# Optimization experiments

Hardware: AMD Instinct MI355X
Metric: run time of the kernel (lower is better)

Reference implementation:

```python
import jax, jax.numpy as jnp
import numpy as np

N, E = 50000, 800000          # nodes, edges
IN, H, C = 256, 4, 64          # in_channels, heads, per-head out channels
HID, OUT = 64, 40              # lin1 hidden, num classes
NEG_SLOPE = 0.2                # PyG GATConv default


def setup_inputs() -> dict:
    key = jax.random.key(0)
    ks = jax.random.split(key, 10)
    s = 0.05
    return {
        "x": jax.random.normal(ks[0], (N, IN), jnp.float32),
        "edge_index": jax.random.randint(ks[1], (2, E), 0, N, dtype=jnp.int64),
        "W": jax.random.normal(ks[2], (IN, H * C), jnp.float32) * s,     # GATConv lin (no bias)
        "att_src": jax.random.normal(ks[3], (H, C), jnp.float32) * s,
        "att_dst": jax.random.normal(ks[4], (H, C), jnp.float32) * s,
        "bias_conv": jnp.zeros((H * C,), jnp.float32),
        "W1": jax.random.normal(ks[5], (H * C, HID), jnp.float32) * s,
        "b1": jnp.zeros((HID,), jnp.float32),
        "W2": jax.random.normal(ks[6], (HID, OUT), jnp.float32) * s,
        "b2": jnp.zeros((OUT,), jnp.float32),
    }


def reference(x, edge_index, W, att_src, att_dst, bias_conv, W1, b1, W2, b2):
    n = x.shape[0]
    # PyG GATConv default: add self-loops (also guarantees no empty segments)
    loop = jnp.arange(n, dtype=edge_index.dtype)
    src = jnp.concatenate([edge_index[0], loop])  # [E+N]
    dst = jnp.concatenate([edge_index[1], loop])

    h = (x @ W).reshape(n, H, C)                         # [N,H,C]
    a_src = jnp.einsum('nhc,hc->nh', h, att_src)         # [N,H]
    a_dst = jnp.einsum('nhc,hc->nh', h, att_dst)

    # per-edge attention logits + segment softmax over incoming edges of dst
    e = jax.nn.leaky_relu(a_src[src] + a_dst[dst], NEG_SLOPE)   # [E+N,H]
    m = jax.ops.segment_max(e, dst, num_segments=n)             # [N,H]
    ex = jnp.exp(e - m[dst])
    denom = jax.ops.segment_sum(ex, dst, num_segments=n)
    alpha = ex / denom[dst]                                     # [E+N,H]

    # weighted scatter-aggregate of source features
    msg = alpha[:, :, None] * h[src]                            # [E+N,H,C]
    out = jax.ops.segment_sum(msg, dst, num_segments=n)         # [N,H,C]
    out = out.reshape(n, H * C) + bias_conv

    out = jax.nn.relu(out)              # .relu() after conv1 (dropout off in eval)
    out = jax.nn.relu(out @ W1 + b1)    # lin1 + relu
    return out @ W2 + b2                # lin2
```

## Files before the change

kernel.cpp:

```cpp
#include <hip/hip_runtime.h>
#include <math.h>

#define HEADS 4
#define CH 64
#define HC 256
#define SLOPE 0.2f
#define SLOT 64

typedef __attribute__((ext_vector_type(8))) short bf16x8;
typedef __attribute__((ext_vector_type(8))) unsigned short u16x8;
typedef __attribute__((ext_vector_type(4))) float f32x4;

__device__ __forceinline__ float4 ld4(const float* p){ return *(const float4*)p; }
__device__ __forceinline__ void st4(float* p, float4 v){ *(float4*)p = v; }
__device__ __forceinline__ float lrelu(float x){ return x > 0.f ? x : SLOPE * x; }
__device__ __forceinline__ unsigned short f2bf(float f){
  union { float f; unsigned int u; } v; v.f = f;
  unsigned int r = v.u + 0x7fffu + ((v.u >> 16) & 1u);
  return (unsigned short)(r >> 16);
}
__device__ __forceinline__ float bflo(unsigned int u){
  union { unsigned int u; float f; } v; v.u = u << 16; return v.f;
}
__device__ __forceinline__ float bfhi(unsigned int u){
  union { unsigned int u; float f; } v; v.u = u & 0xffff0000u; return v.f;
}
__device__ __forceinline__ void split2(float v, unsigned short& h, unsigned short& l){
  unsigned int u = __float_as_uint(v);
  h = (unsigned short)(u >> 16);
  float hf = __uint_as_float(u & 0xffff0000u);
  l = (unsigned short)(__float_as_uint(v - hf) >> 16);
}
__device__ __forceinline__ void dma16(const unsigned short* g, unsigned short* l){
  __builtin_amdgcn_global_load_lds(
      (const __attribute__((address_space(1))) unsigned int*)g,
      (__attribute__((address_space(3))) unsigned int*)l, 16, 0, 0);
}

__global__ __launch_bounds__(256) void k_pre(
    const float* __restrict__ W, const float* __restrict__ W1, const float* __restrict__ W2,
    unsigned short* __restrict__ Bhi, unsigned short* __restrict__ Blo,
    unsigned short* __restrict__ W1h, unsigned short* __restrict__ W1l,
    unsigned short* __restrict__ W2h, unsigned short* __restrict__ W2l) {
  int b = blockIdx.x, t = threadIdx.x;
  if (b < 256) {
    int nn = b;
    unsigned short h, l;
    split2(W[(size_t)t*256 + nn], h, l);
    Bhi[(size_t)nn*256 + t] = h; Blo[(size_t)nn*256 + t] = l;
  } else if (b < 320) {
    int nn = b - 256;
    unsigned short h, l;
    split2(W1[(size_t)t*64 + nn], h, l);
    W1h[(size_t)nn*256 + t] = h; W1l[(size_t)nn*256 + t] = l;
  } else {
    if (t < 64) {
      int nn = b - 320;
      float v = (nn < 40) ? W2[(size_t)t*40 + nn] : 0.f;
      unsigned short h, l;
      split2(v, h, l);
      W2h[(size_t)nn*64 + t] = h; W2l[(size_t)nn*64 + t] = l;
    }
  }
}

__global__ __launch_bounds__(256, 4) void k_gemmfill(const float* __restrict__ x,
    const unsigned short* __restrict__ Bhi_t, const unsigned short* __restrict__ Blo_t,
    unsigned short* __restrict__ hbf,
    const float* __restrict__ att_src, const float* __restrict__ att_dst,
    float* __restrict__ a_srcO, float* __restrict__ a_dstO, int M, int nFill,
    const int* __restrict__ ei, int* __restrict__ cnt, int* __restrict__ csrf,
    int E, int EN) {
  __shared__ __align__(16) unsigned short L[4*4096];
  int t = threadIdx.x;
  int b = blockIdx.x;
  if (b < nFill) {
    int base = b*2048 + t;
    int s0=0,d0=0,s1=0,d1=0,s2=0,d2=0,s3=0,d3=0;
    int s4=0,d4=0,s5=0,d5=0,s6=0,d6=0,s7=0,d7=0;
    int e0=base, e1=base+256, e2=base+512, e3=base+768;
    int e4=base+1024, e5=base+1280, e6=base+1536, e7=base+1792;
    bool q0=e0<EN,q1=e1<EN,q2=e2<EN,q3=e3<EN,q4=e4<EN,q5=e5<EN,q6=e6<EN,q7=e7<EN;
    if (q0) { if (e0<E) { s0=ei[e0]; d0=ei[E+e0]; } else { s0=e0-E; d0=s0; } }
    if (q1) { if (e1<E) { s1=ei[e1]; d1=ei[E+e1]; } else { s1=e1-E; d1=s1; } }
    if (q2) { if (e2<E) { s2=ei[e2]; d2=ei[E+e2]; } else { s2=e2-E; d2=s2; } }
    if (q3) { if (e3<E) { s3=ei[e3]; d3=ei[E+e3]; } else { s3=e3-E; d3=s3; } }
    if (q4) { if (e4<E) { s4=ei[e4]; d4=ei[E+e4]; } else { s4=e4-E; d4=s4; } }
    if (q5) { if (e5<E) { s5=ei[e5]; d5=ei[E+e5]; } else { s5=e5-E; d5=s5; } }
    if (q6) { if (e6<E) { s6=ei[e6]; d6=ei[E+e6]; } else { s6=e6-E; d6=s6; } }
    if (q7) { if (e7<E) { s7=ei[e7]; d7=ei[E+e7]; } else { s7=e7-E; d7=s7; } }
    if (q0) { int p = atomicAdd(&cnt[d0], 1); csrf[(d0<<6) + p] = s0; }
    if (q1) { int p = atomicAdd(&cnt[d1], 1); csrf[(d1<<6) + p] = s1; }
    if (q2) { int p = atomicAdd(&cnt[d2], 1); csrf[(d2<<6) + p] = s2; }
    if (q3) { int p = atomicAdd(&cnt[d3], 1); csrf[(d3<<6) + p] = s3; }
    if (q4) { int p = atomicAdd(&cnt[d4], 1); csrf[(d4<<6) + p] = s4; }
    if (q5) { int p = atomicAdd(&cnt[d5], 1); csrf[(d5<<6) + p] = s5; }
    if (q6) { int p = atomicAdd(&cnt[d6], 1); csrf[(d6<<6) + p] = s6; }
    if (q7) { int p = atomicAdd(&cnt[d7], 1); csrf[(d7<<6) + p] = s7; }
    return;
  }
  int gb = b - nFill;
  int lane = t & 63, w = t >> 6;
  int wr = w >> 1, wc = w & 1;
  int ln15 = lane & 15, lq = lane >> 4;
  int row0 = (gb >> 1) * 128, col0 = (gb & 1) * 128;

  f32x4 acc[4][4];
  #pragma unroll
  for (int i=0;i<4;i++)
    #pragma unroll
    for (int j=0;j<4;j++) acc[i][j] = (f32x4){0.f,0.f,0.f,0.f};

  int sA = w*128 + lane;
  int sB = sA + 64;
  int RA = sA>>3, uA = (sA&7)^(RA&7), idxA = (RA<<1)|(uA&1), segA = uA>>1;
  int RB = sB>>3, uB = (sB&7)^(RB&7), idxB = (RB<<1)|(uB&1), segB = uB>>1;
  size_t gB_a = (size_t)(col0+idxA)*256 + segA*8;
  size_t gB_b = (size_t)(col0+idxB)*256 + segB*8;
  int l0 = (w*128)*8, l1 = (w*128+64)*8;

  int ar = t >> 1, akh = t & 1;
  int arow = row0 + ar;
  bool avalid = arow < M;
  const float* xp = &x[(size_t)arow*256 + akh*16];
  int aR = ar >> 1;
  int u0w = ((2*akh+0) << 1) | (ar & 1);
  int u1w = ((2*akh+1) << 1) | (ar & 1);
  int as0 = aR*8 + (u0w ^ (aR & 7));
  int as1 = aR*8 + (u1w ^ (aR & 7));

  for (int c = 0; c < 8; c++) {
    int k0 = c*32;
    dma16(Bhi_t + gB_a + k0, &L[2*4096 + l0]);
    dma16(Bhi_t + gB_b + k0, &L[2*4096 + l1]);
    dma16(Blo_t + gB_a + k0, &L[3*4096 + l0]);
    dma16(Blo_t + gB_b + k0, &L[3*4096 + l1]);
    float4 f0 = make_float4(0,0,0,0), f1 = f0, f2 = f0, f3 = f0;
    if (avalid) {
      const float* xc = xp + k0;
      f0 = ld4(xc); f1 = ld4(xc+4); f2 = ld4(xc+8); f3 = ld4(xc+12);
    }
    u16x8 h0, l0v, h1, l1v;
    unsigned short hh, ll;
    split2(f0.x,hh,ll); h0[0]=hh; l0v[0]=ll;
    split2(f0.y,hh,ll); h0[1]=hh; l0v[1]=ll;
    split2(f0.z,hh,ll); h0[2]=hh; l0v[2]=ll;
    split2(f0.w,hh,ll); h0[3]=hh; l0v[3]=ll;
    split2(f1.x,hh,ll); h0[4]=hh; l0v[4]=ll;
    split2(f1.y,hh,ll); h0[5]=hh; l0v[5]=ll;
    split2(f1.z,hh,ll); h0[6]=hh; l0v[6]=ll;
    split2(f1.w,hh,ll); h0[7]=hh; l0v[7]=ll;
    split2(f2.x,hh,ll); h1[0]=hh; l1v[0]=ll;
    split2(f2.y,hh,ll); h1[1]=hh; l1v[1]=ll;
    split2(f2.z,hh,ll); h1[2]=hh; l1v[2]=ll;
    split2(f2.w,hh,ll); h1[3]=hh; l1v[3]=ll;
    split2(f3.x,hh,ll); h1[4]=hh; l1v[4]=ll;
    split2(f3.y,hh,ll); h1[5]=hh; l1v[5]=ll;
    split2(f3.z,hh,ll); h1[6]=hh; l1v[6]=ll;
    split2(f3.w,hh,ll); h1[7]=hh; l1v[7]=ll;
    *(u16x8*)&L[0*4096 + as0*8] = h0;
    *(u16x8*)&L[1*4096 + as0*8] = l0v;
    *(u16x8*)&L[0*4096 + as1*8] = h1;
    *(u16x8*)&L[1*4096 + as1*8] = l1v;
    __syncthreads();

    bf16x8 bh[4], bl[4];
    #pragma unroll
    for (int j = 0; j < 4; j++) {
      int nn = wc*64 + j*16 + ln15;
      int R = nn >> 1, u = (lq << 1) | (nn & 1);
      int s = R*8 + (u ^ (R & 7));
      bh[j] = *(bf16x8*)&L[2*4096 + s*8];
      bl[j] = *(bf16x8*)&L[3*4096 + s*8];
    }
    #pragma unroll
    for (int i = 0; i < 4; i++) {
      int r = wr*64 + i*16 + ln15;
      int R = r >> 1, u = (lq << 1) | (r & 1);
      int s = R*8 + (u ^ (R & 7));
      bf16x8 ah = *(bf16x8*)&L[0*4096 + s*8];
      bf16x8 al = *(bf16x8*)&L[1*4096 + s*8];
      #pragma unroll
      for (int j = 0; j < 4; j++) {
        acc[i][j] = __builtin_amdgcn_mfma_f32_16x16x32_bf16(ah, bh[j], acc[i][j], 0,0,0);
        acc[i][j] = __builtin_amdgcn_mfma_f32_16x16x32_bf16(al, bh[j], acc[i][j], 0,0,0);
        acc[i][j] = __builtin_amdgcn_mfma_f32_16x16x32_bf16(ah, bl[j], acc[i][j], 0,0,0);
      }
    }
    __syncthreads();
  }
  unsigned short* hb2 = hbf + (size_t)(gb & 1) * M * 128;
  #pragma unroll
  for (int i = 0; i < 4; i++) {
    #pragma unroll
    for (int r = 0; r < 4; r++) {
      int row = row0 + wr*64 + i*16 + lq*4 + r;
      if (row < M) {
        #pragma unroll
        for (int j = 0; j < 4; j++) {
          int col = wc*64 + j*16 + ln15;
          hb2[(size_t)row*128 + col] = f2bf(acc[i][j][r]);
        }
      }
    }
  }
  int head = (gb & 1)*2 + wc;
  float asv[4], adv[4];
  #pragma unroll
  for (int j=0;j<4;j++){
    asv[j] = att_src[head*CH + j*16 + ln15];
    adv[j] = att_dst[head*CH + j*16 + ln15];
  }
  #pragma unroll
  for (int i = 0; i < 4; i++) {
    #pragma unroll
    for (int r = 0; r < 4; r++) {
      float ps = acc[i][0][r]*asv[0] + acc[i][1][r]*asv[1]
               + acc[i][2][r]*asv[2] + acc[i][3][r]*asv[3];
      float pd = acc[i][0][r]*adv[0] + acc[i][1][r]*adv[1]
               + acc[i][2][r]*adv[2] + acc[i][3][r]*adv[3];
      #pragma unroll
      for (int m=8; m>=1; m>>=1) { ps += __shfl_xor(ps, m); pd += __shfl_xor(pd, m); }
      if (ln15 == 0) {
        int row = row0 + wr*64 + i*16 + lq*4 + r;
        if (row < M) { a_srcO[row*4+head] = ps; a_dstO[row*4+head] = pd; }
      }
    }
  }
}

__global__ __launch_bounds__(256) void k_gat(const unsigned short* __restrict__ hbf,
    const float* __restrict__ a_src, const float* __restrict__ a_dst,
    const int* __restrict__ cnt, const int* __restrict__ csrf,
    const float* __restrict__ bias, unsigned short* __restrict__ outbf,
    int N, int nBlk) {
  int w = threadIdx.x >> 6, lane = threadIdx.x & 63;
  int q = lane >> 4, cl = lane & 15;
  int pass = (blockIdx.x >= nBlk) ? 1 : 0;
  int blk = blockIdx.x - pass*nBlk;
  int n = blk*16 + w*4 + q;
  int c0 = cl * 8;
  int hd = cl >> 3;
  int eb = q * 16;
  const unsigned short* hb = hbf + (size_t)pass * N * 128;
  const int* row = &csrf[(size_t)n << 6];

  __shared__ float s_p[4][64][2];

  float2 ad = *(const float2*)&a_dst[(size_t)n*4 + pass*2];
  float dsum = 0.f;
  float acc[8];
  #pragma unroll
  for (int k=0;k<8;k++) acc[k]=0.f;

  int deg = cnt[n];
  int dm = max(deg, __shfl_xor(deg, 16));
  dm = max(dm, __shfl_xor(dm, 32));

  for (int cb = 0; cb < dm; cb += 16) {
    int cnt16 = min(16, deg - cb);
    int cm  = min(16, dm - cb);
    int s = 0;
    float p0 = 0.f, p1 = 0.f;
    if (cl < cnt16) {
      s = row[cb + cl];
      float2 as = *(const float2*)&a_src[(size_t)s*4 + pass*2];
      p0 = __expf(lrelu(as.x + ad.x));
      p1 = __expf(lrelu(as.y + ad.y));
    }
    *(float2*)&s_p[w][eb + cl][0] = make_float2(p0, p1);

    bool v0 = 0 < cnt16, v1 = 1 < cnt16, v2 = 2 < cnt16, v3 = 3 < cnt16;
    uint4 u0 = make_uint4(0,0,0,0), u1 = u0, u2 = u0, u3 = u0;
    int ss;
    ss = __shfl(s, eb + 0); if (v0) u0 = *(const uint4*)&hb[(size_t)ss*128 + c0];
    ss = __shfl(s, eb + 1); if (v1) u1 = *(const uint4*)&hb[(size_t)ss*128 + c0];
    ss = __shfl(s, eb + 2); if (v2) u2 = *(const uint4*)&hb[(size_t)ss*128 + c0];
    ss = __shfl(s, eb + 3); if (v3) u3 = *(const uint4*)&hb[(size_t)ss*128 + c0];
    for (int g = 0; g < cm; g += 4) {
      int f0 = g+4, f1 = g+5, f2 = g+6, f3 = g+7;
      bool w0 = f0 < cnt16, w1 = f1 < cnt16, w2 = f2 < cnt16, w3 = f3 < cnt16;
      uint4 t0 = make_uint4(0,0,0,0), t1 = t0, t2 = t0, t3 = t0;
      ss = __shfl(s, eb + (f0 & 15)); if (w0) t0 = *(const uint4*)&hb[(size_t)ss*128 + c0];
      ss = __shfl(s, eb + (f1 & 15)); if (w1) t1 = *(const uint4*)&hb[(size_t)ss*128 + c0];
      ss = __shfl(s, eb + (f2 & 15)); if (w2) t2 = *(const uint4*)&hb[(size_t)ss*128 + c0];
      ss = __shfl(s, eb + (f3 & 15)); if (w3) t3 = *(const uint4*)&hb[(size_t)ss*128 + c0];
      if (v0) {
        float pw = s_p[w][eb + g    ][hd]; dsum += pw;
        acc[0] += pw*bflo(u0.x); acc[1] += pw*bfhi(u0.x);
        acc[2] += pw*bflo(u0.y); acc[3] += pw*bfhi(u0.y);
        acc[4] += pw*bflo(u0.z); acc[5] += pw*bfhi(u0.z);
        acc[6] += pw*bflo(u0.w); acc[7] += pw*bfhi(u0.w);
      }
      if (v1) {
        float pw = s_p[w][eb + g + 1][hd]; dsum += pw;
        acc[0] += pw*bflo(u1.x); acc[1] += pw*bfhi(u1.x);
        acc[2] += pw*bflo(u1.y); acc[3] += pw*bfhi(u1.y);
        acc[4] += pw*bflo(u1.z); acc[5] += pw*bfhi(u1.z);
        acc[6] += pw*bflo(u1.w); acc[7] += pw*bfhi(u1.w);
      }
      if (v2) {
        float pw = s_p[w][eb + g + 2][hd]; dsum += pw;
        acc[0] += pw*bflo(u2.x); acc[1] += pw*bfhi(u2.x);
        acc[2] += pw*bflo(u2.y); acc[3] += pw*bfhi(u2.y);
        acc[4] += pw*bflo(u2.z); acc[5] += pw*bfhi(u2.z);
        acc[6] += pw*bflo(u2.w); acc[7] += pw*bfhi(u2.w);
      }
      if (v3) {
        float pw = s_p[w][eb + g + 3][hd]; dsum += pw;
        acc[0] += pw*bflo(u3.x); acc[1] += pw*bfhi(u3.x);
        acc[2] += pw*bflo(u3.y); acc[3] += pw*bfhi(u3.y);
        acc[4] += pw*bflo(u3.z); acc[5] += pw*bfhi(u3.z);
        acc[6] += pw*bflo(u3.w); acc[7] += pw*bfhi(u3.w);
      }
      u0 = t0; u1 = t1; u2 = t2; u3 = t3;
      v0 = w0; v1 = w1; v2 = w2; v3 = w3;
    }
  }
  float inv = 1.f / dsum;
  float4 b0 = ld4(&bias[pass*128 + c0]);
  float4 b1 = ld4(&bias[pass*128 + c0 + 4]);
  uint4 o;
  o.x = (unsigned)f2bf(fmaxf(acc[0]*inv + b0.x, 0.f))
      | ((unsigned)f2bf(fmaxf(acc[1]*inv + b0.y, 0.f)) << 16);
  o.y = (unsigned)f2bf(fmaxf(acc[2]*inv + b0.z, 0.f))
      | ((unsigned)f2bf(fmaxf(acc[3]*inv + b0.w, 0.f)) << 16);
  o.z = (unsigned)f2bf(fmaxf(acc[4]*inv + b1.x, 0.f))
      | ((unsigned)f2bf(fmaxf(acc[5]*inv + b1.y, 0.f)) << 16);
  o.w = (unsigned)f2bf(fmaxf(acc[6]*inv + b1.z, 0.f))
      | ((unsigned)f2bf(fmaxf(acc[7]*inv + b1.w, 0.f)) << 16);
  *(uint4*)&outbf[(size_t)n*HC + pass*128 + c0] = o;
}

__global__ __launch_bounds__(256) void k_mlp(const unsigned short* __restrict__ Cbf,
    const unsigned short* __restrict__ W1h, const unsigned short* __restrict__ W1l,
    const unsigned short* __restrict__ W2h, const unsigned short* __restrict__ W2l,
    const float* __restrict__ b1, const float* __restrict__ b2,
    float* __restrict__ out, int M) {
  __shared__ __align__(16) unsigned short Abuf[4096];
  __shared__ __align__(16) unsigned short Hs[128*72];
  int t = threadIdx.x, lane = t & 63, w = t >> 6;
  int ln15 = lane & 15, lq = lane >> 4;
  int row0 = blockIdx.x * 128;

  f32x4 acc1[2][4];
  #pragma unroll
  for (int i=0;i<2;i++)
    #pragma unroll
    for (int j=0;j<4;j++) acc1[i][j] = (f32x4){0.f,0.f,0.f,0.f};

  int sA = w*64 + lane;
  int sB = 256 + w*64 + lane;
  int rA = sA >> 2, segA = (sA & 3) ^ ((rA >> 1) & 3);
  int rB = sB >> 2, segB = (sB & 3) ^ ((rB >> 1) & 3);
  size_t gA = (size_t)(row0 + rA) * 256 + segA*8;
  size_t gB = (size_t)(row0 + rB) * 256 + segB*8;
  int lA = (w*64)*8, lB = (256 + w*64)*8;

  for (int c = 0; c < 8; c++) {
    int k0 = c*32;
    dma16(Cbf + gA + k0, &Abuf[lA]);
    dma16(Cbf + gB + k0, &Abuf[lB]);
    __syncthreads();
    bf16x8 a[2];
    #pragma unroll
    for (int i = 0; i < 2; i++) {
      int r = w*32 + i*16 + ln15;
      int s = r*4 + (lq ^ ((r >> 1) & 3));
      a[i] = *(bf16x8*)&Abuf[s*8];
    }
    #pragma unroll
    for (int j = 0; j < 4; j++) {
      int n = j*16 + ln15;
      int k = k0 + lq*8;
      bf16x8 bh = *(const bf16x8*)&W1h[(size_t)n*256 + k];
      bf16x8 bl = *(const bf16x8*)&W1l[(size_t)n*256 + k];
      #pragma unroll
      for (int i = 0; i < 2; i++) {
        acc1[i][j] = __builtin_amdgcn_mfma_f32_16x16x32_bf16(a[i], bh, acc1[i][j], 0,0,0);
        acc1[i][j] = __builtin_amdgcn_mfma_f32_16x16x32_bf16(a[i], bl, acc1[i][j], 0,0,0);
      }
    }
    __syncthreads();
  }
  #pragma unroll
  for (int j = 0; j < 4; j++) {
    int col = j*16 + ln15;
    float bv = b1[col];
    #pragma unroll
    for (int i = 0; i < 2; i++) {
      #pragma unroll
      for (int r = 0; r < 4; r++) {
        int row = w*32 + i*16 + lq*4 + r;
        Hs[row*72 + col] = f2bf(fmaxf(acc1[i][j][r] + bv, 0.f));
      }
    }
  }
  f32x4 acc2[2][3];
  #pragma unroll
  for (int i=0;i<2;i++)
    #pragma unroll
    for (int j=0;j<3;j++) acc2[i][j] = (f32x4){0.f,0.f,0.f,0.f};
  #pragma unroll
  for (int kf = 0; kf < 2; kf++) {
    bf16x8 a2[2];
    #pragma unroll
    for (int i = 0; i < 2; i++) {
      int m = w*32 + i*16 + ln15;
      a2[i] = *(bf16x8*)&Hs[m*72 + kf*32 + lq*8];
    }
    #pragma unroll
    for (int j = 0; j < 3; j++) {
      int n = j*16 + ln15;
      int k = kf*32 + lq*8;
      bf16x8 wh = *(const bf16x8*)&W2h[(size_t)n*64 + k];
      bf16x8 wl = *(const bf16x8*)&W2l[(size_t)n*64 + k];
      #pragma unroll
      for (int i = 0; i < 2; i++) {
        acc2[i][j] = __builtin_amdgcn_mfma_f32_16x16x32_bf16(a2[i], wh, acc2[i][j], 0,0,0);
        acc2[i][j] = __builtin_amdgcn_mfma_f32_16x16x32_bf16(a2[i], wl, acc2[i][j], 0,0,0);
      }
    }
  }
  #pragma unroll
  for (int j = 0; j < 3; j++) {
    int col = j*16 + ln15;
    if (col < 40) {
      float bv = b2[col];
      #pragma unroll
      for (int i = 0; i < 2; i++) {
        #pragma unroll
        for (int r = 0; r < 4; r++) {
          int row = row0 + w*32 + i*16 + lq*4 + r;
          if (row < M) out[(size_t)row*40 + col] = acc2[i][j][r] + bv;
        }
      }
    }
  }
}

extern "C" void kernel_launch(void* const* d_in, const int* in_sizes, int n_in,
                              void* d_out, int out_size, void* d_ws, size_t ws_size,
                              hipStream_t stream) {
  const int Nn = in_sizes[0] / HC;
  const int E  = in_sizes[1] / 2;
  const int Mpad = (Nn + 127) & ~127;
  const float* x        = (const float*)d_in[0];
  const int*   ei       = (const int*)d_in[1];
  const float* W        = (const float*)d_in[2];
  const float* att_src  = (const float*)d_in[3];
  const float* att_dst  = (const float*)d_in[4];
  const float* biasconv = (const float*)d_in[5];
  const float* W1       = (const float*)d_in[6];
  const float* b1       = (const float*)d_in[7];
  const float* W2       = (const float*)d_in[8];
  const float* b2       = (const float*)d_in[9];
  float* out = (float*)d_out;

  size_t off = 0;
  auto alloc = [&](size_t bytes)->void* {
    void* p = (void*)((char*)d_ws + off);
    off += (bytes + 255) & ~(size_t)255;
    return p;
  };
  unsigned short* hbf  = (unsigned short*)alloc((size_t)Nn*HC*sizeof(unsigned short));
  unsigned short* outc = (unsigned short*)alloc((size_t)Mpad*HC*sizeof(unsigned short));
  unsigned short* Bhi = (unsigned short*)alloc((size_t)256*256*sizeof(unsigned short));
  unsigned short* Blo = (unsigned short*)alloc((size_t)256*256*sizeof(unsigned short));
  unsigned short* W1h = (unsigned short*)alloc((size_t)64*256*sizeof(unsigned short));
  unsigned short* W1l = (unsigned short*)alloc((size_t)64*256*sizeof(unsigned short));
  unsigned short* W2h = (unsigned short*)alloc((size_t)48*64*sizeof(unsigned short));
  unsigned short* W2l = (unsigned short*)alloc((size_t)48*64*sizeof(unsigned short));
  float* a_src_v  = (float*)alloc((size_t)Nn*4*sizeof(float));
  float* a_dst_v  = (float*)alloc((size_t)Nn*4*sizeof(float));
  int*   cnt      = (int*)alloc((size_t)Nn*sizeof(int));
  int*   csrf     = (int*)alloc((size_t)Nn*SLOT*sizeof(int));
  (void)ws_size; (void)n_in; (void)out_size;

  dim3 blk(256);
  int nGemm = 2 * (Mpad/128);
  int EN = E + Nn;
  int nFill = (EN + 2047)/2048;
  int nBlkGat = Nn/16;

  hipMemsetAsync(cnt, 0, (size_t)Nn*sizeof(int), stream);
  k_pre<<<dim3(368), blk, 0, stream>>>(W, W1, W2,
      Bhi, Blo, W1h, W1l, W2h, W2l);
  k_gemmfill<<<dim3(nFill + nGemm), blk, 0, stream>>>(x, Bhi, Blo, hbf,
      att_src, att_dst, a_src_v, a_dst_v, Nn, nFill, ei, cnt, csrf, E, EN);
  k_gat<<<dim3(2*nBlkGat), blk, 0, stream>>>(hbf, a_src_v, a_dst_v,
                                             cnt, csrf, biasconv, outc, Nn, nBlkGat);
  k_mlp<<<dim3(Mpad/128), blk, 0, stream>>>(outc, W1h, W1l, W2h, W2l, b1, b2, out, Nn);
}
```

Before: 253.3 us.

## Shrink CSR indices to 16-bit, fold count reset into prep, retile MLP

Three unrelated changes. The fixed-slot CSR source indices are stored as 16-bit values to halve their write and read traffic, and the memset of the degree counters moves into extra blocks of the weight-prep kernel so one launch is dropped. The MLP kernel now uses 64-row tiles with A fragments loaded straight from global into registers, replacing the LDS DMA staging loop and its barriers. The 16-bit indices only hold while the node count stays below 65536, so correctness depends on the problem size.

```diff
diff --git a/kernel.cpp b/kernel.cpp
--- a/kernel.cpp
+++ b/kernel.cpp
@@ -41,7 +41,8 @@
     const float* __restrict__ W, const float* __restrict__ W1, const float* __restrict__ W2,
     unsigned short* __restrict__ Bhi, unsigned short* __restrict__ Blo,
     unsigned short* __restrict__ W1h, unsigned short* __restrict__ W1l,
-    unsigned short* __restrict__ W2h, unsigned short* __restrict__ W2l) {
+    unsigned short* __restrict__ W2h, unsigned short* __restrict__ W2l,
+    int* __restrict__ cnt, int Nn) {
   int b = blockIdx.x, t = threadIdx.x;
   if (b < 256) {
     int nn = b;
@@ -53,7 +54,7 @@
     unsigned short h, l;
     split2(W1[(size_t)t*64 + nn], h, l);
     W1h[(size_t)nn*256 + t] = h; W1l[(size_t)nn*256 + t] = l;
-  } else {
+  } else if (b < 368) {
     if (t < 64) {
       int nn = b - 320;
       float v = (nn < 40) ? W2[(size_t)t*40 + nn] : 0.f;
@@ -61,6 +62,9 @@
       split2(v, h, l);
       W2h[(size_t)nn*64 + t] = h; W2l[(size_t)nn*64 + t] = l;
     }
+  } else {
+    int i = (b - 368)*256 + t;
+    if (i < Nn) cnt[i] = 0;
   }
 }
 
@@ -69,7 +73,7 @@
     unsigned short* __restrict__ hbf,
     const float* __restrict__ att_src, const float* __restrict__ att_dst,
     float* __restrict__ a_srcO, float* __restrict__ a_dstO, int M, int nFill,
-    const int* __restrict__ ei, int* __restrict__ cnt, int* __restrict__ csrf,
+    const int* __restrict__ ei, int* __restrict__ cnt, unsigned short* __restrict__ csrf,
     int E, int EN) {
   __shared__ __align__(16) unsigned short L[4*4096];
   int t = threadIdx.x;
@@ -89,14 +93,14 @@
     if (q5) { if (e5<E) { s5=ei[e5]; d5=ei[E+e5]; } else { s5=e5-E; d5=s5; } }
     if (q6) { if (e6<E) { s6=ei[e6]; d6=ei[E+e6]; } else { s6=e6-E; d6=s6; } }
     if (q7) { if (e7<E) { s7=ei[e7]; d7=ei[E+e7]; } else { s7=e7-E; d7=s7; } }
-    if (q0) { int p = atomicAdd(&cnt[d0], 1); csrf[(d0<<6) + p] = s0; }
-    if (q1) { int p = atomicAdd(&cnt[d1], 1); csrf[(d1<<6) + p] = s1; }
-    if (q2) { int p = atomicAdd(&cnt[d2], 1); csrf[(d2<<6) + p] = s2; }
-    if (q3) { int p = atomicAdd(&cnt[d3], 1); csrf[(d3<<6) + p] = s3; }
-    if (q4) { int p = atomicAdd(&cnt[d4], 1); csrf[(d4<<6) + p] = s4; }
-    if (q5) { int p = atomicAdd(&cnt[d5], 1); csrf[(d5<<6) + p] = s5; }
-    if (q6) { int p = atomicAdd(&cnt[d6], 1); csrf[(d6<<6) + p] = s6; }
-    if (q7) { int p = atomicAdd(&cnt[d7], 1); csrf[(d7<<6) + p] = s7; }
+    if (q0) { int p = atomicAdd(&cnt[d0], 1); csrf[(d0<<6) + p] = (unsigned short)s0; }
+    if (q1) { int p = atomicAdd(&cnt[d1], 1); csrf[(d1<<6) + p] = (unsigned short)s1; }
+    if (q2) { int p = atomicAdd(&cnt[d2], 1); csrf[(d2<<6) + p] = (unsigned short)s2; }
+    if (q3) { int p = atomicAdd(&cnt[d3], 1); csrf[(d3<<6) + p] = (unsigned short)s3; }
+    if (q4) { int p = atomicAdd(&cnt[d4], 1); csrf[(d4<<6) + p] = (unsigned short)s4; }
+    if (q5) { int p = atomicAdd(&cnt[d5], 1); csrf[(d5<<6) + p] = (unsigned short)s5; }
+    if (q6) { int p = atomicAdd(&cnt[d6], 1); csrf[(d6<<6) + p] = (unsigned short)s6; }
+    if (q7) { int p = atomicAdd(&cnt[d7], 1); csrf[(d7<<6) + p] = (unsigned short)s7; }
     return;
   }
   int gb = b - nFill;
@@ -231,7 +235,7 @@
 
 __global__ __launch_bounds__(256) void k_gat(const unsigned short* __restrict__ hbf,
     const float* __restrict__ a_src, const float* __restrict__ a_dst,
-    const int* __restrict__ cnt, const int* __restrict__ csrf,
+    const int* __restrict__ cnt, const unsigned short* __restrict__ csrf,
     const float* __restrict__ bias, unsigned short* __restrict__ outbf,
     int N, int nBlk) {
   int w = threadIdx.x >> 6, lane = threadIdx.x & 63;
@@ -243,7 +247,7 @@
   int hd = cl >> 3;
   int eb = q * 16;
   const unsigned short* hb = hbf + (size_t)pass * N * 128;
-  const int* row = &csrf[(size_t)n << 6];
+  const unsigned short* row = &csrf[(size_t)n << 6];
 
   __shared__ float s_p[4][64][2];
 
@@ -337,89 +341,63 @@
     const unsigned short* __restrict__ W2h, const unsigned short* __restrict__ W2l,
     const float* __restrict__ b1, const float* __restrict__ b2,
     float* __restrict__ out, int M) {
-  __shared__ __align__(16) unsigned short Abuf[4096];
-  __shared__ __align__(16) unsigned short Hs[128*72];
+  __shared__ __align__(16) unsigned short Hs[64*72];
   int t = threadIdx.x, lane = t & 63, w = t >> 6;
   int ln15 = lane & 15, lq = lane >> 4;
-  int row0 = blockIdx.x * 128;
-
-  f32x4 acc1[2][4];
-  #pragma unroll
-  for (int i=0;i<2;i++)
-    #pragma unroll
-    for (int j=0;j<4;j++) acc1[i][j] = (f32x4){0.f,0.f,0.f,0.f};
-
-  int sA = w*64 + lane;
-  int sB = 256 + w*64 + lane;
-  int rA = sA >> 2, segA = (sA & 3) ^ ((rA >> 1) & 3);
-  int rB = sB >> 2, segB = (sB & 3) ^ ((rB >> 1) & 3);
-  size_t gA = (size_t)(row0 + rA) * 256 + segA*8;
-  size_t gB = (size_t)(row0 + rB) * 256 + segB*8;
-  int lA = (w*64)*8, lB = (256 + w*64)*8;
-
-  for (int c = 0; c < 8; c++) {
-    int k0 = c*32;
-    dma16(Cbf + gA + k0, &Abuf[lA]);
-    dma16(Cbf + gB + k0, &Abuf[lB]);
-    __syncthreads();
-    bf16x8 a[2];
-    #pragma unroll
-    for (int i = 0; i < 2; i++) {
-      int r = w*32 + i*16 + ln15;
-      int s = r*4 + (lq ^ ((r >> 1) & 3));
-      a[i] = *(bf16x8*)&Abuf[s*8];
-    }
+  int row0 = blockIdx.x * 64;
+  int arow = row0 + w*16 + ln15;
+
+  bf16x8 a[8];
+  bool av = arow < M;
+  const unsigned short* ap = &Cbf[(size_t)arow*256 + lq*8];
+  #pragma unroll
+  for (int kf = 0; kf < 8; kf++) {
+    if (av) a[kf] = *(const bf16x8*)(ap + kf*32);
+    else    a[kf] = (bf16x8){0,0,0,0,0,0,0,0};
+  }
+
+  f32x4 acc1[4];
+  #pragma unroll
+  for (int j=0;j<4;j++) acc1[j] = (f32x4){0.f,0.f,0.f,0.f};
+
+  #pragma unroll
+  for (int kf = 0; kf < 8; kf++) {
+    int k = kf*32 + lq*8;
     #pragma unroll
     for (int j = 0; j < 4; j++) {
       int n = j*16 + ln15;
-      int k = k0 + lq*8;
       bf16x8 bh = *(const bf16x8*)&W1h[(size_t)n*256 + k];
       bf16x8 bl = *(const bf16x8*)&W1l[(size_t)n*256 + k];
-      #pragma unroll
-      for (int i = 0; i < 2; i++) {
-        acc1[i][j] = __builtin_amdgcn_mfma_f32_16x16x32_bf16(a[i], bh, acc1[i][j], 0,0,0);
-        acc1[i][j] = __builtin_amdgcn_mfma_f32_16x16x32_bf16(a[i], bl, acc1[i][j], 0,0,0);
-      }
-    }
-    __syncthreads();
+      acc1[j] = __builtin_amdgcn_mfma_f32_16x16x32_bf16(a[kf], bh, acc1[j], 0,0,0);
+      acc1[j] = __builtin_amdgcn_mfma_f32_16x16x32_bf16(a[kf], bl, acc1[j], 0,0,0);
+    }
   }
   #pragma unroll
   for (int j = 0; j < 4; j++) {
     int col = j*16 + ln15;
     float bv = b1[col];
     #pragma unroll
-    for (int i = 0; i < 2; i++) {
-      #pragma unroll
-      for (int r = 0; r < 4; r++) {
-        int row = w*32 + i*16 + lq*4 + r;
-        Hs[row*72 + col] = f2bf(fmaxf(acc1[i][j][r] + bv, 0.f));
-      }
-    }
-  }
-  f32x4 acc2[2][3];
-  #pragma unroll
-  for (int i=0;i<2;i++)
-    #pragma unroll
-    for (int j=0;j<3;j++) acc2[i][j] = (f32x4){0.f,0.f,0.f,0.f};
+    for (int r = 0; r < 4; r++) {
+      int rl = w*16 + lq*4 + r;
+      Hs[rl*72 + col] = f2bf(fmaxf(acc1[j][r] + bv, 0.f));
+    }
+  }
+  __syncthreads();
+  f32x4 acc2[3];
+  #pragma unroll
+  for (int j=0;j<3;j++) acc2[j] = (f32x4){0.f,0.f,0.f,0.f};
   #pragma unroll
   for (int kf = 0; kf < 2; kf++) {
-    bf16x8 a2[2];
-    #pragma unroll
-    for (int i = 0; i < 2; i++) {
-      int m = w*32 + i*16 + ln15;
-      a2[i] = *(bf16x8*)&Hs[m*72 + kf*32 + lq*8];
-    }
+    int m = w*16 + ln15;
+    bf16x8 a2 = *(bf16x8*)&Hs[m*72 + kf*32 + lq*8];
     #pragma unroll
     for (int j = 0; j < 3; j++) {
       int n = j*16 + ln15;
       int k = kf*32 + lq*8;
       bf16x8 wh = *(const bf16x8*)&W2h[(size_t)n*64 + k];
       bf16x8 wl = *(const bf16x8*)&W2l[(size_t)n*64 + k];
-      #pragma unroll
-      for (int i = 0; i < 2; i++) {
-        acc2[i][j] = __builtin_amdgcn_mfma_f32_16x16x32_bf16(a2[i], wh, acc2[i][j], 0,0,0);
-        acc2[i][j] = __builtin_amdgcn_mfma_f32_16x16x32_bf16(a2[i], wl, acc2[i][j], 0,0,0);
-      }
+      acc2[j] = __builtin_amdgcn_mfma_f32_16x16x32_bf16(a2, wh, acc2[j], 0,0,0);
+      acc2[j] = __builtin_amdgcn_mfma_f32_16x16x32_bf16(a2, wl, acc2[j], 0,0,0);
     }
   }
   #pragma unroll
@@ -428,12 +406,9 @@
     if (col < 40) {
       float bv = b2[col];
       #pragma unroll
-      for (int i = 0; i < 2; i++) {
-        #pragma unroll
-        for (int r = 0; r < 4; r++) {
-          int row = row0 + w*32 + i*16 + lq*4 + r;
-          if (row < M) out[(size_t)row*40 + col] = acc2[i][j][r] + bv;
-        }
+      for (int r = 0; r < 4; r++) {
+        int row = row0 + w*16 + lq*4 + r;
+        if (row < M) out[(size_t)row*40 + col] = acc2[j][r] + bv;
       }
     }
   }
@@ -474,21 +449,21 @@
   float* a_src_v  = (float*)alloc((size_t)Nn*4*sizeof(float));
   float* a_dst_v  = (float*)alloc((size_t)Nn*4*sizeof(float));
   int*   cnt      = (int*)alloc((size_t)Nn*sizeof(int));
-  int*   csrf     = (int*)alloc((size_t)Nn*SLOT*sizeof(int));
+  unsigned short* csrf = (unsigned short*)alloc((size_t)Nn*SLOT*sizeof(unsigned short));
   (void)ws_size; (void)n_in; (void)out_size;
 
   dim3 blk(256);
   int nGemm = 2 * (Mpad/128);
   int EN = E + Nn;
   int nFill = (EN + 2047)/2048;
+  int nZero = (Nn + 255)/256;
   int nBlkGat = Nn/16;
 
-  hipMemsetAsync(cnt, 0, (size_t)Nn*sizeof(int), stream);
-  k_pre<<<dim3(368), blk, 0, stream>>>(W, W1, W2,
-      Bhi, Blo, W1h, W1l, W2h, W2l);
+  k_pre<<<dim3(368 + nZero), blk, 0, stream>>>(W, W1, W2,
+      Bhi, Blo, W1h, W1l, W2h, W2l, cnt, Nn);
   k_gemmfill<<<dim3(nFill + nGemm), blk, 0, stream>>>(x, Bhi, Blo, hbf,
       att_src, att_dst, a_src_v, a_dst_v, Nn, nFill, ei, cnt, csrf, E, EN);
   k_gat<<<dim3(2*nBlkGat), blk, 0, stream>>>(hbf, a_src_v, a_dst_v,
                                              cnt, csrf, biasconv, outc, Nn, nBlkGat);
-  k_mlp<<<dim3(Mpad/128), blk, 0, stream>>>(outc, W1h, W1l, W2h, W2l, b1, b2, out, Nn);
-}
+  k_mlp<<<dim3((Mpad + 63)/64), blk, 0, stream>>>(outc, W1h, W1l, W2h, W2l, b1, b2, out, Nn);
+}
```

After: 267.7 us. 5.7% more time.
